# Optimization experiments

Hardware: AMD Instinct MI355X
Metric: run time of the kernel (lower is better)

The kernel has to match this reference:

```python
import jax, jax.numpy as jnp
import numpy as np

N, E, H, NODE_IN, EDGE_DIM, L = 10000, 400000, 128, 6, 3, 4
LN_EPS = 1e-5


def _lin_init(key, fan_in, fan_out):
    return jax.random.normal(key, (fan_in, fan_out), dtype=jnp.float32) / np.sqrt(fan_in)


def setup_inputs() -> dict:
    key = jax.random.key(0)
    ks = jax.random.split(key, 24)
    x = jax.random.normal(ks[0], (N, NODE_IN), dtype=jnp.float32)
    edge_index = jax.random.randint(ks[1], (2, E), 0, N, dtype=jnp.int64)
    edge_attr = jax.random.normal(ks[2], (E, EDGE_DIM), dtype=jnp.float32)
    # encoder
    enc_w1 = _lin_init(ks[3], NODE_IN, H); enc_b1 = jnp.zeros((H,), jnp.float32)
    enc_w2 = _lin_init(ks[4], H, H); enc_b2 = jnp.zeros((H,), jnp.float32)
    # per-layer stacked params [L, ...]
    msg_w1 = jax.vmap(lambda k: _lin_init(k, 2 * H + EDGE_DIM, H))(jax.random.split(ks[5], L))
    msg_b1 = jnp.zeros((L, H), jnp.float32)
    msg_w2 = jax.vmap(lambda k: _lin_init(k, H, H))(jax.random.split(ks[6], L))
    msg_b2 = jnp.zeros((L, H), jnp.float32)
    upd_w1 = jax.vmap(lambda k: _lin_init(k, 2 * H, H))(jax.random.split(ks[7], L))
    upd_b1 = jnp.zeros((L, H), jnp.float32)
    upd_w2 = jax.vmap(lambda k: _lin_init(k, H, H))(jax.random.split(ks[8], L))
    upd_b2 = jnp.zeros((L, H), jnp.float32)
    ln_g = jnp.ones((L, H), jnp.float32)
    ln_b = jnp.zeros((L, H), jnp.float32)
    # decoder
    dec_w1 = _lin_init(ks[9], H, H); dec_b1 = jnp.zeros((H,), jnp.float32)
    dec_w2 = _lin_init(ks[10], H, 1); dec_b2 = jnp.zeros((1,), jnp.float32)
    return dict(x=x, edge_index=edge_index, edge_attr=edge_attr,
                enc_w1=enc_w1, enc_b1=enc_b1, enc_w2=enc_w2, enc_b2=enc_b2,
                msg_w1=msg_w1, msg_b1=msg_b1, msg_w2=msg_w2, msg_b2=msg_b2,
                upd_w1=upd_w1, upd_b1=upd_b1, upd_w2=upd_w2, upd_b2=upd_b2,
                ln_g=ln_g, ln_b=ln_b,
                dec_w1=dec_w1, dec_b1=dec_b1, dec_w2=dec_w2, dec_b2=dec_b2)


def _layernorm(h, g, b):
    mu = jnp.mean(h, axis=-1, keepdims=True)
    var = jnp.mean(jnp.square(h - mu), axis=-1, keepdims=True)
    return (h - mu) * jax.lax.rsqrt(var + LN_EPS) * g + b


def reference(x, edge_index, edge_attr,
              enc_w1, enc_b1, enc_w2, enc_b2,
              msg_w1, msg_b1, msg_w2, msg_b2,
              upd_w1, upd_b1, upd_w2, upd_b2,
              ln_g, ln_b,
              dec_w1, dec_b1, dec_w2, dec_b2):
    src, tgt = edge_index[0], edge_index[1]  # PyG default flow: message from x_j=src to x_i=tgt
    # in-degree counts for mean aggregation (zero-degree nodes -> 0 output, like scatter_mean)
    counts = jax.ops.segment_sum(jnp.ones((E,), jnp.float32), tgt, num_segments=N)
    inv_counts = (1.0 / jnp.maximum(counts, 1.0))[:, None]
    # encoder
    h = jax.nn.relu(x @ enc_w1 + enc_b1) @ enc_w2 + enc_b2  # [N, H]
    for l in range(L):
        x_i = h[tgt]  # [E, H] target features
        x_j = h[src]  # [E, H] source features
        m_in = jnp.concatenate([x_i, x_j, edge_attr], axis=-1)  # [E, 2H+edge_dim]
        m = jax.nn.relu(m_in @ msg_w1[l] + msg_b1[l]) @ msg_w2[l] + msg_b2[l]  # [E, H]
        agg = jax.ops.segment_sum(m, tgt, num_segments=N) * inv_counts  # [N, H] mean aggregate
        u_in = jnp.concatenate([h, agg], axis=-1)  # [N, 2H]
        u = jax.nn.relu(u_in @ upd_w1[l] + upd_b1[l]) @ upd_w2[l] + upd_b2[l]
        h = _layernorm(u + h, ln_g[l], ln_b[l])  # residual (in==out channels)
    # decoder
    return jax.nn.relu(h @ dec_w1 + dec_b1) @ dec_w2 + dec_b2  # [N, 1]
```

## Files before the change

### kernel.cpp

```cpp
#include <hip/hip_runtime.h>

#define NN 10000
#define NE 400000
#define HD 128
#define NIN 6
#define EDIM 3
#define NL 4
#define CAP 96
#define LN_EPS 1e-5f

typedef unsigned short u16;
using short8 = __attribute__((ext_vector_type(8))) short;
using f32x4 = __attribute__((ext_vector_type(4))) float;

__device__ __forceinline__ u16 f2bf(float x) {
    unsigned u = __float_as_uint(x);
    return (u16)((u + 0x7fff + ((u >> 16) & 1)) >> 16);
}
__device__ __forceinline__ float bf2f(u16 h) { return __uint_as_float(((unsigned)h) << 16); }
__device__ __forceinline__ void split2(float x, u16& hi, u16& lo) {
    hi = f2bf(x);
    lo = f2bf(x - bf2f(hi));
}
#define MFMA(a, b, c) __builtin_amdgcn_mfma_f32_16x16x32_bf16((a), (b), (c), 0, 0, 0)


__global__ __launch_bounds__(256) void k_prepscat(
    const float* __restrict__ msg_w2, const float* __restrict__ msg_b2, const float* __restrict__ upd_w1,
    const float* __restrict__ upd_w2, const float* __restrict__ msg_w1, const float* __restrict__ dec_w1,
    const float* __restrict__ enc_w2, float* __restrict__ c2,
    u16* __restrict__ fG1, u16* __restrict__ fG2, u16* __restrict__ fPQ,
    u16* __restrict__ fDec, u16* __restrict__ fEnc,
    const int* __restrict__ srcp, const int* __restrict__ tgtp, const float* __restrict__ eattr,
    int* __restrict__ cnt, float4* __restrict__ sea) {
    if (blockIdx.x >= 442) {
        int e = (blockIdx.x - 442) * 256 + threadIdx.x;
        if (e < NE) {
            int t = tgtp[e];
            int pos = atomicAdd(&cnt[t], 1);
            if (pos < CAP) {
                sea[t * CAP + pos] = make_float4(eattr[e * 3], eattr[e * 3 + 1], eattr[e * 3 + 2],
                                                 __uint_as_float((unsigned)srcp[e]));
            }
        }
        return;
    }
    int idx = blockIdx.x * 256 + threadIdx.x;
    if (idx < 65536) {
        int l = idx >> 14, rem = idx & 16383, i = rem >> 7, jj = rem & 127;
        const float* U1b = upd_w1 + (size_t)l * 2 * HD * HD + (size_t)HD * HD;
        const float* W2 = msg_w2 + (size_t)l * HD * HD + (size_t)i * HD;
        float acc = 0.f;
        for (int t = 0; t < HD; ++t) acc += W2[t] * U1b[(size_t)t * HD + jj];
        int ct = jj >> 4;
        int ks = 4 + (i >> 5);
        int lane = (((i & 31) >> 3) << 4) | (jj & 15);
        int j = i & 7;
        int g = (l << 12) | (ct << 9) | (ks << 6) | lane;
        fG1[(size_t)g * 8 + j] = f2bf(acc);
    } else if (idx < 66048) {
        int r = idx - 65536;
        int l = r >> 7, jj = r & 127;
        const float* U1b = upd_w1 + (size_t)l * 2 * HD * HD + (size_t)HD * HD;
        const float* b2 = msg_b2 + l * HD;
        float acc = 0.f;
        for (int t = 0; t < HD; ++t) acc += b2[t] * U1b[(size_t)t * HD + jj];
        c2[r] = acc;
    } else if (idx < 76048) {
    } else if (idx < 84240) {
        int gl = idx - 76048;
        int l = gl >> 11, rem = gl & 2047;
        int ct = rem >> 8, ks = (rem >> 6) & 3, lane = rem & 63;
        int n = ct * 16 + (lane & 15), kb = ks * 32 + ((lane >> 4) << 3);
        int g = (l << 12) | (ct << 9) | (ks << 6) | lane;
        u16* dst = fG1 + (size_t)g * 8;
        const float* U = upd_w1 + (size_t)l * 256 * 128;
#pragma unroll
        for (int j = 0; j < 8; ++j) dst[j] = f2bf(U[(size_t)(kb + j) * 128 + n]);
    } else if (idx < 92432) {
        int gg = idx - 84240;
        int l = gg >> 11, r = gg & 2047;
        int ct = r >> 8, ks = (r >> 6) & 3, lane = r & 63;
        int n = ct * 16 + (lane & 15), kb = ks * 32 + ((lane >> 4) << 3);
        u16* dst = fG2 + (size_t)gg * 8;
        const float* W = upd_w2 + (size_t)l * 128 * 128;
#pragma unroll
        for (int j = 0; j < 8; ++j) dst[j] = f2bf(W[(size_t)(kb + j) * 128 + n]);
    } else if (idx < 108816) {
        int gg = idx - 92432;
        int li = gg >> 12, r = gg & 4095;
        int ct = r >> 8, ks = (r >> 6) & 3, lane = r & 63;
        int n = ct * 16 + (lane & 15), kb = ks * 32 + ((lane >> 4) << 3);
        u16* dst = fPQ + (size_t)gg * 8;
        const float* W = msg_w1 + (size_t)li * (2 * HD + EDIM) * HD;
#pragma unroll
        for (int j = 0; j < 8; ++j) {
            int k = kb + j;
            float v = (n < 128) ? W[(size_t)k * 128 + n] : W[(size_t)(128 + k) * 128 + (n - 128)];
            dst[j] = f2bf(v);
        }
    } else if (idx < 110864) {
        int r = idx - 108816;
        int ct = r >> 8, ks = (r >> 6) & 3, lane = r & 63;
        int n = ct * 16 + (lane & 15), kb = ks * 32 + ((lane >> 4) << 3);
        u16* dst = fDec + (size_t)r * 8;
#pragma unroll
        for (int j = 0; j < 8; ++j) dst[j] = f2bf(dec_w1[(size_t)(kb + j) * 128 + n]);
    } else if (idx < 112912) {
        int r = idx - 110864;
        int ct = r >> 8, ks = (r >> 6) & 3, lane = r & 63;
        int n = ct * 16 + (lane & 15), kb = ks * 32 + ((lane >> 4) << 3);
        u16* dst = fEnc + (size_t)r * 8;
#pragma unroll
        for (int j = 0; j < 8; ++j) dst[j] = f2bf(enc_w2[(size_t)(kb + j) * 128 + n]);
    }
}


__global__ __launch_bounds__(512) void k_enc(
    const float* __restrict__ x, const float* __restrict__ ew1, const float* __restrict__ eb1,
    const u16* __restrict__ fEnc, const float* __restrict__ eb2, const u16* __restrict__ fPQ0,
    const float* __restrict__ mb1, u16* __restrict__ h_hi, u16* __restrict__ h_lo,
    float* __restrict__ PQf, u16* __restrict__ Qb) {
    __shared__ u16 tHi[2048], tLo[2048];
    int tid = threadIdx.x, w = tid >> 6, lane = tid & 63, q = lane >> 4, c = lane & 15;
    int band = blockIdx.x * 16;
    {
        int col = w * 16 + c;
        float wv[NIN];
#pragma unroll
        for (int k = 0; k < NIN; ++k) wv[k] = ew1[k * HD + col];
        float ebv = eb1[col];
#pragma unroll
        for (int reg = 0; reg < 4; ++reg) {
            int row = band + q * 4 + reg;
            float t = ebv;
#pragma unroll
            for (int k = 0; k < NIN; ++k) t += x[(size_t)row * NIN + k] * wv[k];
            t = fmaxf(t, 0.f);
            u16 hi, lo;
            split2(t, hi, lo);
            int r16 = q * 4 + reg;
            int a = r16 * 128 + (((col >> 3) ^ r16) << 3) + (col & 7);
            tHi[a] = hi;
            tLo[a] = lo;
        }
    }
    __syncthreads();
    short8 aH[4], aL[4];
#pragma unroll
    for (int ks = 0; ks < 4; ++ks) {
        int a = c * 128 + (((ks * 4 + q) ^ c) << 3);
        aH[ks] = *(const short8*)&tHi[a];
        aL[ks] = *(const short8*)&tLo[a];
    }
    f32x4 acc = {0, 0, 0, 0};
    {
        const u16* fb = fEnc + (size_t)w * 4 * 512 + lane * 8;
#pragma unroll
        for (int ks = 0; ks < 4; ++ks) {
            short8 b = *(const short8*)(fb + ks * 512);
            acc = MFMA(aH[ks], b, acc);
            acc = MFMA(aL[ks], b, acc);
        }
    }
    __syncthreads();
    {
        int col = w * 16 + c;
        float ebv = eb2[col];
#pragma unroll
        for (int reg = 0; reg < 4; ++reg) {
            int r16 = q * 4 + reg, row = band + r16;
            float hval = acc[reg] + ebv;
            u16 hi, lo;
            split2(hval, hi, lo);
            h_hi[(size_t)row * HD + col] = hi;
            h_lo[(size_t)row * HD + col] = lo;
            int a = r16 * 128 + (((col >> 3) ^ r16) << 3) + (col & 7);
            tHi[a] = hi;
            tLo[a] = lo;
        }
    }
    __syncthreads();
#pragma unroll
    for (int ks = 0; ks < 4; ++ks) {
        int a = c * 128 + (((ks * 4 + q) ^ c) << 3);
        aH[ks] = *(const short8*)&tHi[a];
        aL[ks] = *(const short8*)&tLo[a];
    }
#pragma unroll
    for (int i = 0; i < 2; ++i) {
        int ctg = w * 2 + i;
        const u16* fb = fPQ0 + (size_t)ctg * 4 * 512 + lane * 8;
        f32x4 a3 = {0, 0, 0, 0};
#pragma unroll
        for (int ks = 0; ks < 4; ++ks) {
            short8 b = *(const short8*)(fb + ks * 512);
            a3 = MFMA(aH[ks], b, a3);
            a3 = MFMA(aL[ks], b, a3);
        }
        int col = ctg * 16 + c;
        if (ctg < 8) {
            float bias = mb1[col];
#pragma unroll
            for (int reg = 0; reg < 4; ++reg)
                PQf[(size_t)(band + q * 4 + reg) * HD + col] = a3[reg] + bias;
        } else {
            int colq = col - 128;
#pragma unroll
            for (int reg = 0; reg < 4; ++reg)
                Qb[(size_t)(band + q * 4 + reg) * HD + colq] = f2bf(a3[reg]);
        }
    }
}


__global__ __launch_bounds__(256) void k_gath(
    const float* __restrict__ PQf_in, const u16* __restrict__ Qb_in,
    const int* __restrict__ cnt, const float4* __restrict__ sea,
    const float* __restrict__ wc, u16* __restrict__ agg_hi, u16* __restrict__ agg_lo) {
    int w = threadIdx.x >> 6, lane = threadIdx.x & 63;
    int n = __builtin_amdgcn_readfirstlane(blockIdx.x * 4 + w);
    int cn = cnt[n];
    int cle = __builtin_amdgcn_readfirstlane(cn < CAP ? cn : CAP);
    int j = lane * 2;
    float2 p = *(const float2*)(PQf_in + (size_t)n * HD + j);
    float2 wcr0 = *(const float2*)(wc + j);
    float2 wcr1 = *(const float2*)(wc + HD + j);
    float2 wcr2 = *(const float2*)(wc + 2 * HD + j);
    const float4* bk = sea + (size_t)n * CAP;
    float e0 = 0.f, e1 = 0.f, o0 = 0.f, o1 = 0.f;
    float4 A0[8], A1[8];
    unsigned U0[8], U1[8];

    auto LA = [&](float4* A, int b) {
#pragma unroll
        for (int k = 0; k < 8; ++k) A[k] = bk[b * 8 + k];
    };
    auto IU = [&](unsigned* U, const float4* A) {
#pragma unroll
        for (int k = 0; k < 8; ++k)
            U[k] = *(const unsigned*)(Qb_in + (size_t)__float_as_uint(A[k].w) * HD + j);
    };
    auto CO = [&](const float4* A, const unsigned* U) {
#pragma unroll
        for (int k = 0; k < 8; ++k) {
            float c0 = A[k].x * wcr0.x + A[k].y * wcr1.x + A[k].z * wcr2.x;
            float c1 = A[k].x * wcr0.y + A[k].y * wcr1.y + A[k].z * wcr2.y;
            float t0 = fmaxf(p.x + __uint_as_float(U[k] << 16) + c0, 0.f);
            float t1 = fmaxf(p.y + __uint_as_float(U[k] & 0xffff0000u) + c1, 0.f);
            if (k & 1) { o0 += t0; o1 += t1; } else { e0 += t0; e1 += t1; }
        }
    };

    int nb = cle >> 3;
    int b = 0;
    if (nb) {
        LA(A0, 0);
        IU(U0, A0);
        for (; b + 2 <= nb; b += 2) {
            LA(A1, b + 1);
            IU(U1, A1);
            CO(A0, U0);
            if (b + 2 < nb) { LA(A0, b + 2); IU(U0, A0); }
            CO(A1, U1);
        }
        if (b < nb) { CO(A0, U0); ++b; }
    }
    int e = nb * 8;
    int rem = cle - e;
    if (rem) {
#pragma unroll
        for (int k = 0; k < 8; ++k) A0[k] = bk[e + (k < rem ? k : 0)];
        IU(U0, A0);
#pragma unroll
        for (int k = 0; k < 8; ++k) {
            float c0 = A0[k].x * wcr0.x + A0[k].y * wcr1.x + A0[k].z * wcr2.x;
            float c1 = A0[k].x * wcr0.y + A0[k].y * wcr1.y + A0[k].z * wcr2.y;
            float t0 = fmaxf(p.x + __uint_as_float(U0[k] << 16) + c0, 0.f);
            float t1 = fmaxf(p.y + __uint_as_float(U0[k] & 0xffff0000u) + c1, 0.f);
            t0 = (k < rem) ? t0 : 0.f;
            t1 = (k < rem) ? t1 : 0.f;
            if (k & 1) { o0 += t0; o1 += t1; } else { e0 += t0; e1 += t1; }
        }
    }
    float invn = 1.0f / fmaxf((float)cn, 1.0f);
    float v0 = (e0 + o0) * invn, v1 = (e1 + o1) * invn;
    u16 h0, l0, h1, l1;
    split2(v0, h0, l0);
    split2(v1, h1, l1);
    *(ushort2*)(agg_hi + (size_t)n * HD + j) = make_ushort2(h0, h1);
    *(ushort2*)(agg_lo + (size_t)n * HD + j) = make_ushort2(l0, l1);
}


template <bool LAST>
__global__ __launch_bounds__(512) void k_layer(
    const u16* __restrict__ agg_hi, const u16* __restrict__ agg_lo, const int* __restrict__ cnt,
    u16* __restrict__ h_hi, u16* __restrict__ h_lo,
    const u16* __restrict__ fG1, const u16* __restrict__ fG2,
    const float* __restrict__ ub1, const float* __restrict__ c2l, const float* __restrict__ ub2,
    const float* __restrict__ g, const float* __restrict__ bb,
    const u16* __restrict__ fPQ, const float* __restrict__ nb1,
    float* __restrict__ PQf_out, u16* __restrict__ Qb_out,
    const u16* __restrict__ fDec, const float* __restrict__ db1, const float* __restrict__ dw2,
    const float* __restrict__ db2, float* __restrict__ out) {
    __shared__ u16 tHi[2048], tLo[2048];
    __shared__ float red[16][8][2];
    int tid = threadIdx.x, w = tid >> 6, lane = tid & 63, q = lane >> 4, c = lane & 15;
    int band = blockIdx.x * 16;
    short8 aH[8], aL[8];
    {
        size_t rb = (size_t)(band + c) * HD + q * 8;
#pragma unroll
        for (int ks = 0; ks < 4; ++ks) {
            aH[ks] = *(const short8*)(h_hi + rb + ks * 32);
            aL[ks] = *(const short8*)(h_lo + rb + ks * 32);
            aH[4 + ks] = *(const short8*)(agg_hi + rb + ks * 32);
            aL[4 + ks] = *(const short8*)(agg_lo + rb + ks * 32);
        }
    }
    f32x4 accA = {0, 0, 0, 0}, accB = {0, 0, 0, 0};
    {
        const u16* fb = fG1 + (size_t)w * 8 * 512 + lane * 8;
#pragma unroll
        for (int ks = 0; ks < 4; ++ks) {
            short8 bA = *(const short8*)(fb + ks * 512);
            short8 bB = *(const short8*)(fb + (ks + 4) * 512);
            accA = MFMA(aH[ks], bA, accA);
            accB = MFMA(aH[ks + 4], bB, accB);
            accA = MFMA(aL[ks], bA, accA);
            accB = MFMA(aL[ks + 4], bB, accB);
        }
    }
    f32x4 acc = accA + accB;
    float alv[4];
#pragma unroll
    for (int reg = 0; reg < 4; ++reg) alv[reg] = (cnt[band + q * 4 + reg] > 0) ? 1.f : 0.f;
    {
        int col = w * 16 + c;
        float u1b = ub1[col], cc = c2l[col];
#pragma unroll
        for (int reg = 0; reg < 4; ++reg) {
            int r16 = q * 4 + reg;
            float t = fmaxf(acc[reg] + u1b + alv[reg] * cc, 0.f);
            u16 hi, lo;
            split2(t, hi, lo);
            int a = r16 * 128 + (((col >> 3) ^ r16) << 3) + (col & 7);
            tHi[a] = hi;
            tLo[a] = lo;
        }
    }
    __syncthreads();
    short8 aH2[4], aL2[4];
#pragma unroll
    for (int ks = 0; ks < 4; ++ks) {
        int a = c * 128 + (((ks * 4 + q) ^ c) << 3);
        aH2[ks] = *(const short8*)&tHi[a];
        aL2[ks] = *(const short8*)&tLo[a];
    }
    f32x4 acc2A = {0, 0, 0, 0}, acc2B = {0, 0, 0, 0};
    {
        const u16* fb = fG2 + (size_t)w * 4 * 512 + lane * 8;
#pragma unroll
        for (int ks = 0; ks < 2; ++ks) {
            short8 bA = *(const short8*)(fb + ks * 512);
            short8 bB = *(const short8*)(fb + (ks + 2) * 512);
            acc2A = MFMA(aH2[ks], bA, acc2A);
            acc2B = MFMA(aH2[ks + 2], bB, acc2B);
            acc2A = MFMA(aL2[ks], bA, acc2A);
            acc2B = MFMA(aL2[ks + 2], bB, acc2B);
        }
    }
    f32x4 acc2 = acc2A + acc2B;
    float vv[4];
    {
        int col = w * 16 + c;
        float u2b = ub2[col];
#pragma unroll
        for (int reg = 0; reg < 4; ++reg) {
            size_t idx = (size_t)(band + q * 4 + reg) * HD + col;
            float hres = bf2f(h_hi[idx]) + bf2f(h_lo[idx]);
            vv[reg] = acc2[reg] + u2b + hres;
        }
    }
#pragma unroll
    for (int reg = 0; reg < 4; ++reg) {
        float s = vv[reg];
        float s2 = vv[reg] * vv[reg];
        for (int m = 1; m < 16; m <<= 1) {
            s += __shfl_xor(s, m);
            s2 += __shfl_xor(s2, m);
        }
        if (c == 0) {
            red[q * 4 + reg][w][0] = s;
            red[q * 4 + reg][w][1] = s2;
        }
    }
    __syncthreads();
    float mu[4], rs[4];
#pragma unroll
    for (int reg = 0; reg < 4; ++reg) {
        int r16 = q * 4 + reg;
        float S1 = 0.f, S2 = 0.f;
#pragma unroll
        for (int ww = 0; ww < 8; ++ww) {
            S1 += red[r16][ww][0];
            S2 += red[r16][ww][1];
        }
        float m = S1 * (1.f / HD);
        float var = S2 * (1.f / HD) - m * m;
        mu[reg] = m;
        rs[reg] = rsqrtf(var + LN_EPS);
    }
    {
        int col = w * 16 + c;
        float gg = g[col], bv = bb[col];
#pragma unroll
        for (int reg = 0; reg < 4; ++reg) {
            int r16 = q * 4 + reg;
            float o = (vv[reg] - mu[reg]) * rs[reg] * gg + bv;
            u16 hi, lo;
            split2(o, hi, lo);
            int a = r16 * 128 + (((col >> 3) ^ r16) << 3) + (col & 7);
            tHi[a] = hi;
            tLo[a] = lo;
            if (!LAST) {
                size_t idx = (size_t)(band + r16) * HD + col;
                h_hi[idx] = hi;
                h_lo[idx] = lo;
            }
        }
    }
    __syncthreads();
    short8 aH3[4], aL3[4];
#pragma unroll
    for (int ks = 0; ks < 4; ++ks) {
        int a = c * 128 + (((ks * 4 + q) ^ c) << 3);
        aH3[ks] = *(const short8*)&tHi[a];
        aL3[ks] = *(const short8*)&tLo[a];
    }
    if (!LAST) {
#pragma unroll
        for (int i = 0; i < 2; ++i) {
            int ctg = w * 2 + i;
            const u16* fb = fPQ + (size_t)ctg * 4 * 512 + lane * 8;
            f32x4 a3A = {0, 0, 0, 0}, a3B = {0, 0, 0, 0};
#pragma unroll
            for (int ks = 0; ks < 2; ++ks) {
                short8 bA = *(const short8*)(fb + ks * 512);
                short8 bB = *(const short8*)(fb + (ks + 2) * 512);
                a3A = MFMA(aH3[ks], bA, a3A);
                a3B = MFMA(aH3[ks + 2], bB, a3B);
                a3A = MFMA(aL3[ks], bA, a3A);
                a3B = MFMA(aL3[ks + 2], bB, a3B);
            }
            f32x4 a3 = a3A + a3B;
            int col = ctg * 16 + c;
            if (ctg < 8) {
                float bias = nb1[col];
#pragma unroll
                for (int reg = 0; reg < 4; ++reg)
                    PQf_out[(size_t)(band + q * 4 + reg) * HD + col] = a3[reg] + bias;
            } else {
                int colq = col - 128;
#pragma unroll
                for (int reg = 0; reg < 4; ++reg)
                    Qb_out[(size_t)(band + q * 4 + reg) * HD + colq] = f2bf(a3[reg]);
            }
        }
    } else {
        float part[4];
        {
            const u16* fb = fDec + (size_t)w * 4 * 512 + lane * 8;
            f32x4 a3A = {0, 0, 0, 0}, a3B = {0, 0, 0, 0};
#pragma unroll
            for (int ks = 0; ks < 2; ++ks) {
                short8 bA = *(const short8*)(fb + ks * 512);
                short8 bB = *(const short8*)(fb + (ks + 2) * 512);
                a3A = MFMA(aH3[ks], bA, a3A);
                a3B = MFMA(aH3[ks + 2], bB, a3B);
                a3A = MFMA(aL3[ks], bA, a3A);
                a3B = MFMA(aL3[ks + 2], bB, a3B);
            }
            f32x4 a3 = a3A + a3B;
            int col = w * 16 + c;
            float w2v = dw2[col], b1v = db1[col];
#pragma unroll
            for (int reg = 0; reg < 4; ++reg) part[reg] = fmaxf(a3[reg] + b1v, 0.f) * w2v;
        }
#pragma unroll
        for (int reg = 0; reg < 4; ++reg) {
            float s = part[reg];
            for (int m = 1; m < 16; m <<= 1) s += __shfl_xor(s, m);
            if (c == 0) red[q * 4 + reg][w][0] = s;
        }
        __syncthreads();
        if (tid < 16) {
            float s = db2[0];
#pragma unroll
            for (int ww = 0; ww < 8; ++ww) s += red[tid][ww][0];
            out[band + tid] = s;
        }
    }
}


extern "C" void kernel_launch(void* const* d_in, const int* in_sizes, int n_in,
                              void* d_out, int out_size, void* d_ws, size_t ws_size,
                              hipStream_t stream) {
    const float* x = (const float*)d_in[0];
    const int* eidx = (const int*)d_in[1];
    const float* eattr = (const float*)d_in[2];
    const float* enc_w1 = (const float*)d_in[3];
    const float* enc_b1 = (const float*)d_in[4];
    const float* enc_w2 = (const float*)d_in[5];
    const float* enc_b2 = (const float*)d_in[6];
    const float* msg_w1 = (const float*)d_in[7];
    const float* msg_b1 = (const float*)d_in[8];
    const float* msg_w2 = (const float*)d_in[9];
    const float* msg_b2 = (const float*)d_in[10];
    const float* upd_w1 = (const float*)d_in[11];
    const float* upd_b1 = (const float*)d_in[12];
    const float* upd_w2 = (const float*)d_in[13];
    const float* upd_b2 = (const float*)d_in[14];
    const float* ln_g = (const float*)d_in[15];
    const float* ln_b = (const float*)d_in[16];
    const float* dec_w1 = (const float*)d_in[17];
    const float* dec_b1 = (const float*)d_in[18];
    const float* dec_w2 = (const float*)d_in[19];
    const float* dec_b2 = (const float*)d_in[20];
    const int* srcp = eidx;
    const int* tgtp = eidx + NE;

    char* base = (char*)d_ws;
    size_t off = 0;
    auto alloc = [&](size_t bytes) -> void* {
        off = (off + 15) & ~(size_t)15;
        void* p = base + off;
        off += bytes;
        return p;
    };
    float4* sea = (float4*)alloc((size_t)NN * CAP * 16);
    float* PQf0 = (float*)alloc((size_t)NN * HD * 4);
    float* PQf1 = (float*)alloc((size_t)NN * HD * 4);
    u16* Qb0 = (u16*)alloc((size_t)NN * HD * 2);
    u16* Qb1 = (u16*)alloc((size_t)NN * HD * 2);
    u16* h_hi = (u16*)alloc((size_t)NN * HD * 2);
    u16* h_lo = (u16*)alloc((size_t)NN * HD * 2);
    u16* agg_hi = (u16*)alloc((size_t)NN * HD * 2);
    u16* agg_lo = (u16*)alloc((size_t)NN * HD * 2);
    int* cnt = (int*)alloc((size_t)NN * 4);
    float* c2 = (float*)alloc((size_t)NL * HD * 4);
    u16* fG1 = (u16*)alloc((size_t)131072 * 2);
    u16* fG2 = (u16*)alloc((size_t)65536 * 2);
    u16* fPQ = (u16*)alloc((size_t)131072 * 2);
    u16* fDec = (u16*)alloc((size_t)16384 * 2);
    u16* fEnc = (u16*)alloc((size_t)16384 * 2);

    hipMemsetAsync(cnt, 0, (size_t)NN * 4, stream);
    k_prepscat<<<442 + (NE + 255) / 256, 256, 0, stream>>>(
        msg_w2, msg_b2, upd_w1, upd_w2, msg_w1, dec_w1, enc_w2,
        c2, fG1, fG2, fPQ, fDec, fEnc,
        srcp, tgtp, eattr, cnt, sea);
    k_enc<<<625, 512, 0, stream>>>(x, enc_w1, enc_b1, fEnc, enc_b2, fPQ,
                                   msg_b1, h_hi, h_lo, PQf0, Qb0);

    float* PQin = PQf0;
    u16* Qin = Qb0;
    float* PQout = PQf1;
    u16* Qout = Qb1;
    for (int l = 0; l < NL; ++l) {
        const float* wc = msg_w1 + (size_t)l * (2 * HD + EDIM) * HD + (size_t)2 * HD * HD;
        k_gath<<<NN / 4, 256, 0, stream>>>(PQin, Qin, cnt, sea, wc, agg_hi, agg_lo);
        if (l < NL - 1) {
            k_layer<false><<<NN / 16, 512, 0, stream>>>(
                agg_hi, agg_lo, cnt, h_hi, h_lo,
                fG1 + (size_t)l * 32768, fG2 + (size_t)l * 16384,
                upd_b1 + l * HD, c2 + l * HD, upd_b2 + l * HD, ln_g + l * HD, ln_b + l * HD,
                fPQ + (size_t)(l + 1) * 32768, msg_b1 + (size_t)(l + 1) * HD, PQout, Qout,
                nullptr, nullptr, nullptr, nullptr, nullptr);
        } else {
            k_layer<true><<<NN / 16, 512, 0, stream>>>(
                agg_hi, agg_lo, cnt, h_hi, h_lo,
                fG1 + (size_t)l * 32768, fG2 + (size_t)l * 16384,
                upd_b1 + l * HD, c2 + l * HD, upd_b2 + l * HD, ln_g + l * HD, ln_b + l * HD,
                nullptr, nullptr, nullptr, nullptr,
                fDec, dec_b1, dec_w2, dec_b2, (float*)d_out);
        }
        float* tf = PQin; PQin = PQout; PQout = tf;
        u16* tq = Qin; Qin = Qout; Qout = tq;
    }
}
```

Measured before the change: 302.5 us.

## Fuse edge gather-aggregation into per-layer update kernel via LDS

Removes the separate k_gath launch and folds the per-node edge aggregation into the start of k_layer. Each wave aggregates two of the block's 16 nodes and writes the split bf16 hi/lo results into swizzled shared memory, and the MFMA A-operands are then read from LDS instead of global agg buffers. This saves one kernel launch per layer and the global write and read of the aggregate arrays. The cost is that the layer kernel now runs only 625 blocks of 512 threads for the latency-bound gather, whereas k_gath used 2500 blocks. It also uses more shared memory and registers, which may reduce occupancy and latency hiding.

```diff
diff --git a/kernel.cpp b/kernel.cpp
--- a/kernel.cpp
+++ b/kernel.cpp
@@ -215,88 +215,10 @@
 }
 
 
-__global__ __launch_bounds__(256) void k_gath(
-    const float* __restrict__ PQf_in, const u16* __restrict__ Qb_in,
-    const int* __restrict__ cnt, const float4* __restrict__ sea,
-    const float* __restrict__ wc, u16* __restrict__ agg_hi, u16* __restrict__ agg_lo) {
-    int w = threadIdx.x >> 6, lane = threadIdx.x & 63;
-    int n = __builtin_amdgcn_readfirstlane(blockIdx.x * 4 + w);
-    int cn = cnt[n];
-    int cle = __builtin_amdgcn_readfirstlane(cn < CAP ? cn : CAP);
-    int j = lane * 2;
-    float2 p = *(const float2*)(PQf_in + (size_t)n * HD + j);
-    float2 wcr0 = *(const float2*)(wc + j);
-    float2 wcr1 = *(const float2*)(wc + HD + j);
-    float2 wcr2 = *(const float2*)(wc + 2 * HD + j);
-    const float4* bk = sea + (size_t)n * CAP;
-    float e0 = 0.f, e1 = 0.f, o0 = 0.f, o1 = 0.f;
-    float4 A0[8], A1[8];
-    unsigned U0[8], U1[8];
-
-    auto LA = [&](float4* A, int b) {
-#pragma unroll
-        for (int k = 0; k < 8; ++k) A[k] = bk[b * 8 + k];
-    };
-    auto IU = [&](unsigned* U, const float4* A) {
-#pragma unroll
-        for (int k = 0; k < 8; ++k)
-            U[k] = *(const unsigned*)(Qb_in + (size_t)__float_as_uint(A[k].w) * HD + j);
-    };
-    auto CO = [&](const float4* A, const unsigned* U) {
-#pragma unroll
-        for (int k = 0; k < 8; ++k) {
-            float c0 = A[k].x * wcr0.x + A[k].y * wcr1.x + A[k].z * wcr2.x;
-            float c1 = A[k].x * wcr0.y + A[k].y * wcr1.y + A[k].z * wcr2.y;
-            float t0 = fmaxf(p.x + __uint_as_float(U[k] << 16) + c0, 0.f);
-            float t1 = fmaxf(p.y + __uint_as_float(U[k] & 0xffff0000u) + c1, 0.f);
-            if (k & 1) { o0 += t0; o1 += t1; } else { e0 += t0; e1 += t1; }
-        }
-    };
-
-    int nb = cle >> 3;
-    int b = 0;
-    if (nb) {
-        LA(A0, 0);
-        IU(U0, A0);
-        for (; b + 2 <= nb; b += 2) {
-            LA(A1, b + 1);
-            IU(U1, A1);
-            CO(A0, U0);
-            if (b + 2 < nb) { LA(A0, b + 2); IU(U0, A0); }
-            CO(A1, U1);
-        }
-        if (b < nb) { CO(A0, U0); ++b; }
-    }
-    int e = nb * 8;
-    int rem = cle - e;
-    if (rem) {
-#pragma unroll
-        for (int k = 0; k < 8; ++k) A0[k] = bk[e + (k < rem ? k : 0)];
-        IU(U0, A0);
-#pragma unroll
-        for (int k = 0; k < 8; ++k) {
-            float c0 = A0[k].x * wcr0.x + A0[k].y * wcr1.x + A0[k].z * wcr2.x;
-            float c1 = A0[k].x * wcr0.y + A0[k].y * wcr1.y + A0[k].z * wcr2.y;
-            float t0 = fmaxf(p.x + __uint_as_float(U0[k] << 16) + c0, 0.f);
-            float t1 = fmaxf(p.y + __uint_as_float(U0[k] & 0xffff0000u) + c1, 0.f);
-            t0 = (k < rem) ? t0 : 0.f;
-            t1 = (k < rem) ? t1 : 0.f;
-            if (k & 1) { o0 += t0; o1 += t1; } else { e0 += t0; e1 += t1; }
-        }
-    }
-    float invn = 1.0f / fmaxf((float)cn, 1.0f);
-    float v0 = (e0 + o0) * invn, v1 = (e1 + o1) * invn;
-    u16 h0, l0, h1, l1;
-    split2(v0, h0, l0);
-    split2(v1, h1, l1);
-    *(ushort2*)(agg_hi + (size_t)n * HD + j) = make_ushort2(h0, h1);
-    *(ushort2*)(agg_lo + (size_t)n * HD + j) = make_ushort2(l0, l1);
-}
-
-
 template <bool LAST>
 __global__ __launch_bounds__(512) void k_layer(
-    const u16* __restrict__ agg_hi, const u16* __restrict__ agg_lo, const int* __restrict__ cnt,
+    const float* __restrict__ PQf_in, const u16* __restrict__ Qb_in,
+    const int* __restrict__ cnt, const float4* __restrict__ sea, const float* __restrict__ wc,
     u16* __restrict__ h_hi, u16* __restrict__ h_lo,
     const u16* __restrict__ fG1, const u16* __restrict__ fG2,
     const float* __restrict__ ub1, const float* __restrict__ c2l, const float* __restrict__ ub2,
@@ -305,10 +227,90 @@
     float* __restrict__ PQf_out, u16* __restrict__ Qb_out,
     const u16* __restrict__ fDec, const float* __restrict__ db1, const float* __restrict__ dw2,
     const float* __restrict__ db2, float* __restrict__ out) {
+    __shared__ u16 sHi[2048], sLo[2048];
     __shared__ u16 tHi[2048], tLo[2048];
     __shared__ float red[16][8][2];
     int tid = threadIdx.x, w = tid >> 6, lane = tid & 63, q = lane >> 4, c = lane & 15;
     int band = blockIdx.x * 16;
+    int j = lane * 2;
+    {
+        float2 wcr0 = *(const float2*)(wc + j);
+        float2 wcr1 = *(const float2*)(wc + HD + j);
+        float2 wcr2 = *(const float2*)(wc + 2 * HD + j);
+#pragma unroll
+        for (int i = 0; i < 2; ++i) {
+            int r16 = w * 2 + i;
+            int n = __builtin_amdgcn_readfirstlane(band + r16);
+            int cn = cnt[n];
+            int cle = __builtin_amdgcn_readfirstlane(cn < CAP ? cn : CAP);
+            float2 p = *(const float2*)(PQf_in + (size_t)n * HD + j);
+            const float4* bk = sea + (size_t)n * CAP;
+            float e0 = 0.f, e1 = 0.f, o0 = 0.f, o1 = 0.f;
+            float4 A0[8], A1[8];
+            unsigned U0[8], U1[8];
+
+            auto LA = [&](float4* A, int b) {
+#pragma unroll
+                for (int k = 0; k < 8; ++k) A[k] = bk[b * 8 + k];
+            };
+            auto IU = [&](unsigned* U, const float4* A) {
+#pragma unroll
+                for (int k = 0; k < 8; ++k)
+                    U[k] = *(const unsigned*)(Qb_in + (size_t)__float_as_uint(A[k].w) * HD + j);
+            };
+            auto CO = [&](const float4* A, const unsigned* U) {
+#pragma unroll
+                for (int k = 0; k < 8; ++k) {
+                    float c0 = A[k].x * wcr0.x + A[k].y * wcr1.x + A[k].z * wcr2.x;
+                    float c1 = A[k].x * wcr0.y + A[k].y * wcr1.y + A[k].z * wcr2.y;
+                    float t0 = fmaxf(p.x + __uint_as_float(U[k] << 16) + c0, 0.f);
+                    float t1 = fmaxf(p.y + __uint_as_float(U[k] & 0xffff0000u) + c1, 0.f);
+                    if (k & 1) { o0 += t0; o1 += t1; } else { e0 += t0; e1 += t1; }
+                }
+            };
+
+            int nb = cle >> 3;
+            int b = 0;
+            if (nb) {
+                LA(A0, 0);
+                IU(U0, A0);
+                for (; b + 2 <= nb; b += 2) {
+                    LA(A1, b + 1);
+                    IU(U1, A1);
+                    CO(A0, U0);
+                    if (b + 2 < nb) { LA(A0, b + 2); IU(U0, A0); }
+                    CO(A1, U1);
+                }
+                if (b < nb) { CO(A0, U0); ++b; }
+            }
+            int e = nb * 8;
+            int rem = cle - e;
+            if (rem) {
+#pragma unroll
+                for (int k = 0; k < 8; ++k) A0[k] = bk[e + (k < rem ? k : 0)];
+                IU(U0, A0);
+#pragma unroll
+                for (int k = 0; k < 8; ++k) {
+                    float c0 = A0[k].x * wcr0.x + A0[k].y * wcr1.x + A0[k].z * wcr2.x;
+                    float c1 = A0[k].x * wcr0.y + A0[k].y * wcr1.y + A0[k].z * wcr2.y;
+                    float t0 = fmaxf(p.x + __uint_as_float(U0[k] << 16) + c0, 0.f);
+                    float t1 = fmaxf(p.y + __uint_as_float(U0[k] & 0xffff0000u) + c1, 0.f);
+                    t0 = (k < rem) ? t0 : 0.f;
+                    t1 = (k < rem) ? t1 : 0.f;
+                    if (k & 1) { o0 += t0; o1 += t1; } else { e0 += t0; e1 += t1; }
+                }
+            }
+            float invn = 1.0f / fmaxf((float)cn, 1.0f);
+            float v0 = (e0 + o0) * invn, v1 = (e1 + o1) * invn;
+            u16 h0, l0, h1, l1;
+            split2(v0, h0, l0);
+            split2(v1, h1, l1);
+            int a = r16 * 128 + (((j >> 3) ^ r16) << 3) + (j & 7);
+            *(ushort2*)&sHi[a] = make_ushort2(h0, h1);
+            *(ushort2*)&sLo[a] = make_ushort2(l0, l1);
+        }
+    }
+    __syncthreads();
     short8 aH[8], aL[8];
     {
         size_t rb = (size_t)(band + c) * HD + q * 8;
@@ -316,8 +318,9 @@
         for (int ks = 0; ks < 4; ++ks) {
             aH[ks] = *(const short8*)(h_hi + rb + ks * 32);
             aL[ks] = *(const short8*)(h_lo + rb + ks * 32);
-            aH[4 + ks] = *(const short8*)(agg_hi + rb + ks * 32);
-            aL[4 + ks] = *(const short8*)(agg_lo + rb + ks * 32);
+            int a = c * 128 + (((ks * 4 + q) ^ c) << 3);
+            aH[4 + ks] = *(const short8*)&sHi[a];
+            aL[4 + ks] = *(const short8*)&sLo[a];
         }
     }
     f32x4 accA = {0, 0, 0, 0}, accB = {0, 0, 0, 0};
@@ -548,8 +551,6 @@
     u16* Qb1 = (u16*)alloc((size_t)NN * HD * 2);
     u16* h_hi = (u16*)alloc((size_t)NN * HD * 2);
     u16* h_lo = (u16*)alloc((size_t)NN * HD * 2);
-    u16* agg_hi = (u16*)alloc((size_t)NN * HD * 2);
-    u16* agg_lo = (u16*)alloc((size_t)NN * HD * 2);
     int* cnt = (int*)alloc((size_t)NN * 4);
     float* c2 = (float*)alloc((size_t)NL * HD * 4);
     u16* fG1 = (u16*)alloc((size_t)131072 * 2);
@@ -572,17 +573,16 @@
     u16* Qout = Qb1;
     for (int l = 0; l < NL; ++l) {
         const float* wc = msg_w1 + (size_t)l * (2 * HD + EDIM) * HD + (size_t)2 * HD * HD;
-        k_gath<<<NN / 4, 256, 0, stream>>>(PQin, Qin, cnt, sea, wc, agg_hi, agg_lo);
         if (l < NL - 1) {
             k_layer<false><<<NN / 16, 512, 0, stream>>>(
-                agg_hi, agg_lo, cnt, h_hi, h_lo,
+                PQin, Qin, cnt, sea, wc, h_hi, h_lo,
                 fG1 + (size_t)l * 32768, fG2 + (size_t)l * 16384,
                 upd_b1 + l * HD, c2 + l * HD, upd_b2 + l * HD, ln_g + l * HD, ln_b + l * HD,
                 fPQ + (size_t)(l + 1) * 32768, msg_b1 + (size_t)(l + 1) * HD, PQout, Qout,
                 nullptr, nullptr, nullptr, nullptr, nullptr);
         } else {
             k_layer<true><<<NN / 16, 512, 0, stream>>>(
-                agg_hi, agg_lo, cnt, h_hi, h_lo,
+                PQin, Qin, cnt, sea, wc, h_hi, h_lo,
                 fG1 + (size_t)l * 32768, fG2 + (size_t)l * 16384,
                 upd_b1 + l * HD, c2 + l * HD, upd_b2 + l * HD, ln_g + l * HD, ln_b + l * HD,
                 nullptr, nullptr, nullptr, nullptr,
```

After: 286.7 us. 5.2% less time.
